# Kernel tuning notes

Hardware: AMD Instinct MI355X
Metric: run time of the kernel (lower is better)

The kernel has to match this reference:

```python
import jax, jax.numpy as jnp
import numpy as np

D_MODEL = 128
EXPAND = 8
D_INNER = EXPAND * D_MODEL            # 1024
HEADDIM = D_MODEL                     # headdim = int(in_channels*8/8)
NHEADS = D_INNER // HEADDIM           # 8
D_STATE = 128
D_CONV = 4
CONV_DIM = D_INNER + 2 * D_STATE      # 1280
D_IN_PROJ = 2 * D_INNER + 2 * D_STATE + NHEADS  # 2312
EPS = 1e-5
B_SZ, SEQ = 2, 2048


def setup_inputs() -> dict:
    key = jax.random.key(0)
    ks = jax.random.split(key, 16)
    n = jax.random.normal
    dt_init = jax.random.uniform(ks[4], (NHEADS,), minval=0.001, maxval=0.1)
    return dict(
        hidden_states=n(ks[0], (B_SZ, SEQ, D_MODEL), jnp.float32),
        w_in=n(ks[1], (D_IN_PROJ, D_MODEL), jnp.float32) / np.float32(np.sqrt(D_MODEL)),
        conv_w=n(ks[2], (CONV_DIM, D_CONV), jnp.float32) / np.float32(np.sqrt(D_CONV)),
        conv_b=n(ks[3], (CONV_DIM,), jnp.float32) * 0.01,
        dt_bias=jnp.log(jnp.expm1(dt_init)),  # inverse-softplus init (official)
        A_log=jnp.log(jax.random.uniform(ks[5], (NHEADS,), minval=1.0, maxval=16.0)),
        D_skip=jnp.ones((NHEADS,), jnp.float32),
        gnorm_w=jnp.ones((D_INNER,), jnp.float32),
        w_out=n(ks[6], (D_MODEL, D_INNER), jnp.float32) / np.float32(np.sqrt(D_INNER)),
        ln1_w=jnp.ones((D_MODEL,), jnp.float32),
        ln1_b=jnp.zeros((D_MODEL,), jnp.float32),
        ln2_w=jnp.ones((D_MODEL,), jnp.float32),
        ln2_b=jnp.zeros((D_MODEL,), jnp.float32),
        mlp_w=n(ks[7], (D_MODEL, D_MODEL), jnp.float32) / np.float32(np.sqrt(D_MODEL)),
        mlp_b=jnp.zeros((D_MODEL,), jnp.float32),
    )


def _layer_norm(x, w, b):
    m = x.mean(-1, keepdims=True)
    xc = x - m
    v = (xc * xc).mean(-1, keepdims=True)
    return xc * jax.lax.rsqrt(v + EPS) * w + b


def _mixer(u, w_in, conv_w, conv_b, dt_bias, A_log, D_skip, gnorm_w, w_out):
    b, l, _ = u.shape
    zxbcdt = u @ w_in.T                                    # (b,l,2312)
    z = zxbcdt[..., :D_INNER]                              # gate
    xBC = zxbcdt[..., D_INNER:D_INNER + CONV_DIM]
    dt = jax.nn.softplus(zxbcdt[..., -NHEADS:] + dt_bias)  # (b,l,h)
    # depthwise causal conv1d + SiLU
    xc = jnp.pad(xBC.swapaxes(1, 2), ((0, 0), (0, 0), (D_CONV - 1, 0)))
    xc = jax.lax.conv_general_dilated(xc, conv_w[:, None, :], (1,), 'VALID',
                                      feature_group_count=CONV_DIM)
    xBC = jax.nn.silu((xc + conv_b[None, :, None]).swapaxes(1, 2))
    x = xBC[..., :D_INNER].reshape(b, l, NHEADS, HEADDIM)  # (b,l,h,p)
    Bm = xBC[..., D_INNER:D_INNER + D_STATE]               # (b,l,n), ngroups=1
    Cm = xBC[..., D_INNER + D_STATE:]                      # (b,l,n)
    A = -jnp.exp(A_log)                                    # (h,)
    dA = jnp.exp(dt * A)                                   # (b,l,h)

    def step(S, inp):
        dA_t, dt_t, B_t, C_t, x_t = inp
        S = S * dA_t[:, :, None, None] + jnp.einsum('bh,bhp,bn->bhpn', dt_t, x_t, B_t)
        return S, jnp.einsum('bhpn,bn->bhp', S, C_t)

    S0 = jnp.zeros((b, NHEADS, HEADDIM, D_STATE), u.dtype)
    _, ys = jax.lax.scan(step, S0, (dA.swapaxes(0, 1), dt.swapaxes(0, 1),
                                    Bm.swapaxes(0, 1), Cm.swapaxes(0, 1),
                                    x.swapaxes(0, 1)))
    y = ys.swapaxes(0, 1) + D_skip[None, None, :, None] * x  # skip connection
    y = y.reshape(b, l, D_INNER) * jax.nn.silu(z)            # gated RMSNorm
    y = y * jax.lax.rsqrt((y * y).mean(-1, keepdims=True) + EPS) * gnorm_w
    return y @ w_out.T


def reference(hidden_states, w_in, conv_w, conv_b, dt_bias, A_log, D_skip,
              gnorm_w, w_out, ln1_w, ln1_b, ln2_w, ln2_b, mlp_w, mlp_b):
    residual = hidden_states
    h = _layer_norm(residual, ln1_w, ln1_b)
    h = _mixer(h, w_in, conv_w, conv_b, dt_bias, A_log, D_skip, gnorm_w, w_out)
    residual = h + residual
    h = _layer_norm(residual, ln2_w, ln2_b)
    return h @ mlp_w.T + mlp_b
```

## Files before the change

### kernel.cpp

```cpp
#include <hip/hip_runtime.h>
#include <hip/hip_bf16.h>

#define B_SZ 2
#define SEQ 2048
#define DMODEL 128
#define DINNER 1024
#define NHEADS 8
#define HEADDIM 128
#define DSTATE 128
#define CONVDIM 1280
#define NPROJ 2304
#define NTOK (B_SZ*SEQ)
#define CHUNK 64
#define NCHUNK (SEQ/CHUNK)
#define LDT 72

using bf16_t = __hip_bfloat16;
using short8 = __attribute__((ext_vector_type(8))) short;
using short4v= __attribute__((ext_vector_type(4))) short;
using f32x4  = __attribute__((ext_vector_type(4))) float;

__device__ __forceinline__ float silu_f(float x) { return x / (1.f + expf(-x)); }
__device__ __forceinline__ float bf2f(short s) {
    unsigned u = ((unsigned)(unsigned short)s) << 16;
    return __uint_as_float(u);
}
__device__ __forceinline__ short f2bf_s(float f) {
    bf16_t h = __float2bfloat16(f);
    return *(short*)&h;
}

__global__ __launch_bounds__(128) void head_fused(
        const float* __restrict__ hidden,
        const float* __restrict__ ln1_w, const float* __restrict__ ln1_b,
        const float* __restrict__ w_in,
        const float* __restrict__ dt_bias, const float* __restrict__ A_log,
        bf16_t* __restrict__ h_bf, float* __restrict__ dtb, float* __restrict__ ldAb,
        const float* __restrict__ wa, int na, const float* __restrict__ wb, int nb,
        const float* __restrict__ wc, int nc,
        bf16_t* __restrict__ oa, bf16_t* __restrict__ ob, bf16_t* __restrict__ oc) {
    int blk = blockIdx.x;
    if (blk >= NTOK) {
        int i = (blk - NTOK) * 128 + threadIdx.x;
        if (i < na) oa[i] = __float2bfloat16(wa[i]);
        else if (i < na + nb) ob[i - na] = __float2bfloat16(wb[i - na]);
        else if (i < na + nb + nc) oc[i - na - nb] = __float2bfloat16(wc[i - na - nb]);
        return;
    }
    int m = blk, t = threadIdx.x;
    __shared__ float red[128];
    __shared__ float sred[2][8];
    float v = hidden[(size_t)m*DMODEL + t];
    red[t] = v; __syncthreads();
    for (int s = 64; s > 0; s >>= 1) { if (t < s) red[t] += red[t+s]; __syncthreads(); }
    float mean = red[0] * (1.f/128.f);
    __syncthreads();
    float xc = v - mean;
    red[t] = xc * xc; __syncthreads();
    for (int s = 64; s > 0; s >>= 1) { if (t < s) red[t] += red[t+s]; __syncthreads(); }
    float var = red[0] * (1.f/128.f);
    float o = xc * rsqrtf(var + 1e-5f) * ln1_w[t] + ln1_b[t];
    h_bf[(size_t)m*DMODEL + t] = __float2bfloat16(o);
    int wave = t >> 6, lane = t & 63;
#pragma unroll
    for (int hd = 0; hd < NHEADS; hd++) {
        float p = o * w_in[(size_t)(NPROJ + hd)*DMODEL + t];
#pragma unroll
        for (int d = 1; d < 64; d <<= 1) p += __shfl_xor(p, d, 64);
        if (lane == 0) sred[wave][hd] = p;
    }
    __syncthreads();
    if (t < NHEADS) {
        float s = sred[0][t] + sred[1][t] + dt_bias[t];
        float dtv = (s > 20.f) ? s : log1pf(expf(s));
        float Av = -expf(A_log[t]);
        dtb[m*NHEADS + t] = dtv;
        ldAb[m*NHEADS + t] = dtv * Av;
    }
}

__global__ __launch_bounds__(256) void gemm_bf(const bf16_t* __restrict__ A,
                                               const bf16_t* __restrict__ W,
                                               bf16_t* __restrict__ C,
                                               int M, int N, int K) {
    int tid = threadIdx.x;
    int wave = tid >> 6, lane = tid & 63;
    int m0 = blockIdx.x * 64 + wave * 16;
    int n0 = blockIdx.y * 64;
    int lr = lane & 15, quad = lane >> 4;
    f32x4 acc[4];
#pragma unroll
    for (int j = 0; j < 4; j++) acc[j] = (f32x4){0.f, 0.f, 0.f, 0.f};
    for (int k0 = 0; k0 < K; k0 += 32) {
        short8 a = *(const short8*)(A + (size_t)(m0 + lr)*K + k0 + quad*8);
#pragma unroll
        for (int j = 0; j < 4; j++) {
            short8 b = *(const short8*)(W + (size_t)(n0 + j*16 + lr)*K + k0 + quad*8);
            acc[j] = __builtin_amdgcn_mfma_f32_16x16x32_bf16(a, b, acc[j], 0, 0, 0);
        }
    }
#pragma unroll
    for (int j = 0; j < 4; j++)
#pragma unroll
        for (int r = 0; r < 4; r++) {
            int row = m0 + quad*4 + r;
            int col = n0 + j*16 + lr;
            C[(size_t)row*N + col] = __float2bfloat16(acc[j][r]);
        }
}

__global__ __launch_bounds__(256) void conv_silu(const bf16_t* __restrict__ zxb,
                                                 const float* __restrict__ conv_w,
                                                 const float* __restrict__ conv_b,
                                                 bf16_t* __restrict__ xBCb) {
    int idx = blockIdx.x * 256 + threadIdx.x;
    if (idx >= NTOK * CONVDIM / 4) return;
    int c4 = (idx % (CONVDIM/4)) * 4;
    int m  = idx / (CONVDIM/4);
    int b = m >> 11, l = m & (SEQ - 1);
    float acc[4];
    f32x4 wv[4];
#pragma unroll
    for (int j = 0; j < 4; j++) {
        acc[j] = conv_b[c4 + j];
        wv[j] = *(const f32x4*)(conv_w + (c4 + j)*4);
    }
#pragma unroll
    for (int k = 0; k < 4; k++) {
        int ll = l - 3 + k;
        if (ll >= 0) {
            short4v v = *(const short4v*)(zxb + (size_t)(b*SEQ + ll)*NPROJ + DINNER + c4);
#pragma unroll
            for (int j = 0; j < 4; j++) acc[j] += bf2f(v[j]) * wv[j][k];
        }
    }
    short4v res;
#pragma unroll
    for (int j = 0; j < 4; j++) res[j] = f2bf_s(silu_f(acc[j]));
    *(short4v*)(xBCb + (size_t)m*CONVDIM + c4) = res;
}

__global__ __launch_bounds__(256) void scanA_mfma(const bf16_t* __restrict__ xBCb,
                                                  const float* __restrict__ dt,
                                                  const float* __restrict__ ldA,
                                                  bf16_t* __restrict__ Sloc,
                                                  float* __restrict__ Pbuf) {
    int bid = blockIdx.x;
    int c = bid & 31, hd = (bid >> 5) & 7, b = bid >> 8;
    int t = threadIdx.x, wave = t >> 6, lane = t & 63;
    int lr = lane & 15, quad = lane >> 4;
    __shared__ bf16_t XT[128*LDT];
    __shared__ bf16_t BT[128*LDT];
    __shared__ float ws[CHUNK];
    int m0tok = b*SEQ + c*CHUNK;
    if (t < 64) {
        float L = ldA[(m0tok + t)*NHEADS + hd];
#pragma unroll
        for (int d = 1; d < 64; d <<= 1) {
            float u = __shfl_up(L, d, 64);
            if (lane >= d) L += u;
        }
        float Ltot = __shfl(L, 63, 64);
        ws[t] = expf(Ltot - L) * dt[(m0tok + t)*NHEADS + hd];
        if (t == 63) Pbuf[bid] = expf(Ltot);
    }
    __syncthreads();
#pragma unroll 4
    for (int i = 0; i < 32; i++) {
        int idx = i*256 + t;
        int tt = idx >> 7, p = idx & 127;
        const bf16_t* row = xBCb + (size_t)(m0tok + tt)*CONVDIM;
        float xv = bf2f(*(const short*)&row[hd*HEADDIM + p]);
        XT[p*LDT + tt] = __float2bfloat16(xv * ws[tt]);
        BT[p*LDT + tt] = row[DINNER + p];
    }
    __syncthreads();
    int m0w = wave * 32;
    f32x4 acc[2][8];
#pragma unroll
    for (int mi = 0; mi < 2; mi++)
#pragma unroll
        for (int ni = 0; ni < 8; ni++) acc[mi][ni] = (f32x4){0.f,0.f,0.f,0.f};
#pragma unroll
    for (int k0 = 0; k0 < 64; k0 += 32) {
        short8 a[2];
#pragma unroll
        for (int mi = 0; mi < 2; mi++)
            a[mi] = *(const short8*)&XT[(m0w + mi*16 + lr)*LDT + k0 + quad*8];
#pragma unroll
        for (int ni = 0; ni < 8; ni++) {
            short8 bb = *(const short8*)&BT[(ni*16 + lr)*LDT + k0 + quad*8];
#pragma unroll
            for (int mi = 0; mi < 2; mi++)
                acc[mi][ni] = __builtin_amdgcn_mfma_f32_16x16x32_bf16(a[mi], bb, acc[mi][ni], 0, 0, 0);
        }
    }
    bf16_t* outp = Sloc + (size_t)bid * 16384;
#pragma unroll
    for (int mi = 0; mi < 2; mi++)
#pragma unroll
        for (int ni = 0; ni < 8; ni++)
#pragma unroll
            for (int r = 0; r < 4; r++) {
                int p = m0w + mi*16 + quad*4 + r;
                int n = ni*16 + lr;
                outp[p*128 + n] = __float2bfloat16(acc[mi][ni][r]);
            }
}

__global__ __launch_bounds__(256) void scanB(const bf16_t* __restrict__ Sloc,
                                             bf16_t* __restrict__ Sini,
                                             const float* __restrict__ Pbuf) {
    int bid = blockIdx.x;
    int bh = bid >> 5, slice = bid & 31;
    int t = threadIdx.x;
    int off = slice*512 + t*2;
    size_t base = (size_t)bh * NCHUNK * 16384;
    float run0 = 0.f, run1 = 0.f;
    for (int cc = 0; cc < NCHUNK; cc++) {
        unsigned raw = *(const unsigned*)(Sloc + base + (size_t)cc*16384 + off);
        float P = Pbuf[bh*NCHUNK + cc];
        unsigned o0 = (unsigned)(unsigned short)f2bf_s(run0);
        unsigned o1 = (unsigned)(unsigned short)f2bf_s(run1);
        *(unsigned*)(Sini + base + (size_t)cc*16384 + off) = o0 | (o1 << 16);
        run0 = run0*P + bf2f((short)(raw & 0xffff));
        run1 = run1*P + bf2f((short)(raw >> 16));
    }
}

__global__ __launch_bounds__(256) void scanC_mfma(const bf16_t* __restrict__ xBCb,
                                                  const float* __restrict__ dt,
                                                  const float* __restrict__ ldA,
                                                  const bf16_t* __restrict__ Sini,
                                                  const float* __restrict__ Dskip,
                                                  float* __restrict__ ybuf) {
    int bid = blockIdx.x;
    int c = bid & 31, hd = (bid >> 5) & 7, b = bid >> 8;
    int t = threadIdx.x, wave = t >> 6, lane = t & 63;
    int lr = lane & 15, quad = lane >> 4;
    __shared__ bf16_t XT[128*LDT];
    __shared__ bf16_t Mlds[64*LDT];
    __shared__ float Ls[CHUNK], dts[CHUNK];
    int m0tok = b*SEQ + c*CHUNK;
    if (t < 64) {
        float L = ldA[(m0tok + t)*NHEADS + hd];
#pragma unroll
        for (int d = 1; d < 64; d <<= 1) {
            float u = __shfl_up(L, d, 64);
            if (lane >= d) L += u;
        }
        Ls[t] = L;
        dts[t] = dt[(m0tok + t)*NHEADS + hd];
    }
#pragma unroll 4
    for (int i = 0; i < 32; i++) {
        int idx = i*256 + t;
        int tt = idx >> 7, p = idx & 127;
        XT[p*LDT + tt] = xBCb[(size_t)(m0tok + tt)*CONVDIM + hd*HEADDIM + p];
    }
    __syncthreads();
    const bf16_t* Crow = xBCb + (size_t)m0tok*CONVDIM + DINNER + DSTATE;
    const bf16_t* Brow = xBCb + (size_t)m0tok*CONVDIM + DINNER;
    f32x4 g[4];
#pragma unroll
    for (int si = 0; si < 4; si++) g[si] = (f32x4){0.f,0.f,0.f,0.f};
#pragma unroll
    for (int k0 = 0; k0 < 128; k0 += 32) {
        short8 a = *(const short8*)(Crow + (size_t)(wave*16 + lr)*CONVDIM + k0 + quad*8);
#pragma unroll
        for (int si = 0; si < 4; si++) {
            short8 bb = *(const short8*)(Brow + (size_t)(si*16 + lr)*CONVDIM + k0 + quad*8);
            g[si] = __builtin_amdgcn_mfma_f32_16x16x32_bf16(a, bb, g[si], 0, 0, 0);
        }
    }
#pragma unroll
    for (int si = 0; si < 4; si++)
#pragma unroll
        for (int r = 0; r < 4; r++) {
            int tt = wave*16 + quad*4 + r;
            int ss = si*16 + lr;
            float v = (ss <= tt) ? g[si][r] * expf(Ls[tt] - Ls[ss]) * dts[ss] : 0.f;
            Mlds[tt*LDT + ss] = __float2bfloat16(v);
        }
    __syncthreads();
    int p0 = wave * 32;
    f32x4 acc[4][2];
#pragma unroll
    for (int mi = 0; mi < 4; mi++)
#pragma unroll
        for (int ni = 0; ni < 2; ni++) acc[mi][ni] = (f32x4){0.f,0.f,0.f,0.f};
    const bf16_t* Sb = Sini + (size_t)bid * 16384;
#pragma unroll
    for (int k0 = 0; k0 < 128; k0 += 32) {
        short8 aC[4];
#pragma unroll
        for (int mi = 0; mi < 4; mi++)
            aC[mi] = *(const short8*)(Crow + (size_t)(mi*16 + lr)*CONVDIM + k0 + quad*8);
#pragma unroll
        for (int ni = 0; ni < 2; ni++) {
            short8 bb = *(const short8*)(Sb + (size_t)(p0 + ni*16 + lr)*128 + k0 + quad*8);
#pragma unroll
            for (int mi = 0; mi < 4; mi++)
                acc[mi][ni] = __builtin_amdgcn_mfma_f32_16x16x32_bf16(aC[mi], bb, acc[mi][ni], 0, 0, 0);
        }
    }
#pragma unroll
    for (int mi = 0; mi < 4; mi++) {
        float el[4];
#pragma unroll
        for (int r = 0; r < 4; r++) el[r] = expf(Ls[mi*16 + quad*4 + r]);
#pragma unroll
        for (int ni = 0; ni < 2; ni++)
#pragma unroll
            for (int r = 0; r < 4; r++) acc[mi][ni][r] *= el[r];
    }
#pragma unroll
    for (int k0 = 0; k0 < 64; k0 += 32) {
        short8 aM[4];
#pragma unroll
        for (int mi = 0; mi < 4; mi++)
            aM[mi] = *(const short8*)&Mlds[(mi*16 + lr)*LDT + k0 + quad*8];
#pragma unroll
        for (int ni = 0; ni < 2; ni++) {
            short8 bb = *(const short8*)&XT[(p0 + ni*16 + lr)*LDT + k0 + quad*8];
#pragma unroll
            for (int mi = 0; mi < 4; mi++)
                acc[mi][ni] = __builtin_amdgcn_mfma_f32_16x16x32_bf16(aM[mi], bb, acc[mi][ni], 0, 0, 0);
        }
    }
    float dsk = Dskip[hd];
#pragma unroll
    for (int mi = 0; mi < 4; mi++)
#pragma unroll
        for (int ni = 0; ni < 2; ni++)
#pragma unroll
            for (int r = 0; r < 4; r++) {
                int tt = mi*16 + quad*4 + r;
                int pp = p0 + ni*16 + lr;
                float xv = bf2f(*(const short*)&XT[pp*LDT + tt]);
                int m = m0tok + tt;
                ybuf[(size_t)m*DINNER + hd*HEADDIM + pp] = acc[mi][ni][r] + dsk*xv;
            }
}

__global__ __launch_bounds__(256) void gate_out(const float* __restrict__ ybuf,
                                                const bf16_t* __restrict__ zxb,
                                                const float* __restrict__ gw,
                                                const bf16_t* __restrict__ Wb,
                                                float* __restrict__ mix) {
    int blk = blockIdx.x, t = threadIdx.x;
    int tok0 = blk * 16;
    int tt = t >> 4, cg = t & 15;
    int ch0 = cg * 64;
    __shared__ bf16_t A[16*1032];
    float vals[64];
    const float*  yr = ybuf + (size_t)(tok0 + tt)*DINNER + ch0;
    const bf16_t* zr = zxb  + (size_t)(tok0 + tt)*NPROJ  + ch0;
    float ss = 0.f;
#pragma unroll
    for (int i = 0; i < 64; i += 4) {
        f32x4 y = *(const f32x4*)(yr + i);
        short4v z = *(const short4v*)(zr + i);
#pragma unroll
        for (int r = 0; r < 4; r++) {
            float v = y[r] * silu_f(bf2f(z[r]));
            vals[i + r] = v; ss += v*v;
        }
    }
#pragma unroll
    for (int d = 1; d < 16; d <<= 1) ss += __shfl_xor(ss, d, 64);
    float rstd = rsqrtf(ss*(1.f/1024.f) + 1e-5f);
#pragma unroll
    for (int i = 0; i < 64; i += 4) {
        short4v pk;
#pragma unroll
        for (int r = 0; r < 4; r++) pk[r] = f2bf_s(vals[i+r]*rstd*gw[ch0+i+r]);
        *(short4v*)&A[tt*1032 + ch0 + i] = pk;
    }
    __syncthreads();
    int wave = t >> 6, lane = t & 63, lr = lane & 15, quad = lane >> 4;
    f32x4 acc[2];
    acc[0] = (f32x4){0.f,0.f,0.f,0.f}; acc[1] = (f32x4){0.f,0.f,0.f,0.f};
    for (int k0 = 0; k0 < 1024; k0 += 32) {
        short8 a = *(const short8*)&A[lr*1032 + k0 + quad*8];
#pragma unroll
        for (int j = 0; j < 2; j++) {
            int col = wave*32 + j*16 + lr;
            short8 bb = *(const short8*)(Wb + (size_t)col*DINNER + k0 + quad*8);
            acc[j] = __builtin_amdgcn_mfma_f32_16x16x32_bf16(a, bb, acc[j], 0, 0, 0);
        }
    }
#pragma unroll
    for (int j = 0; j < 2; j++)
#pragma unroll
        for (int r = 0; r < 4; r++) {
            int row = tok0 + quad*4 + r;
            int col = wave*32 + j*16 + lr;
            mix[(size_t)row*DMODEL + col] = acc[j][r];
        }
}

__global__ __launch_bounds__(256) void ln_mlp(const float* __restrict__ mix,
                                              const float* __restrict__ resid,
                                              const float* __restrict__ w,
                                              const float* __restrict__ b,
                                              const bf16_t* __restrict__ Wm,
                                              const float* __restrict__ mb,
                                              float* __restrict__ out) {
    int blk = blockIdx.x, t = threadIdx.x;
    int tok0 = blk * 16;
    int tt = t >> 4, cg = t & 15;
    int ch0 = cg * 8;
    __shared__ bf16_t A[16*136];
    const float* xr = mix   + (size_t)(tok0 + tt)*DMODEL + ch0;
    const float* rr = resid + (size_t)(tok0 + tt)*DMODEL + ch0;
    float v[8];
    {
        f32x4 x0 = *(const f32x4*)xr, x1 = *(const f32x4*)(xr + 4);
        f32x4 r0 = *(const f32x4*)rr, r1 = *(const f32x4*)(rr + 4);
#pragma unroll
        for (int r = 0; r < 4; r++) { v[r] = x0[r] + r0[r]; v[4+r] = x1[r] + r1[r]; }
    }
    float s = 0.f, sq = 0.f;
#pragma unroll
    for (int i = 0; i < 8; i++) { s += v[i]; sq += v[i]*v[i]; }
#pragma unroll
    for (int d = 1; d < 16; d <<= 1) { s += __shfl_xor(s, d, 64); sq += __shfl_xor(sq, d, 64); }
    float mean = s * (1.f/128.f);
    float var  = sq * (1.f/128.f) - mean*mean;
    float rstd = rsqrtf(var + 1e-5f);
    {
        short4v p0, p1;
#pragma unroll
        for (int r = 0; r < 4; r++) {
            p0[r] = f2bf_s((v[r]   - mean)*rstd*w[ch0+r]   + b[ch0+r]);
            p1[r] = f2bf_s((v[4+r] - mean)*rstd*w[ch0+4+r] + b[ch0+4+r]);
        }
        *(short4v*)&A[tt*136 + ch0]     = p0;
        *(short4v*)&A[tt*136 + ch0 + 4] = p1;
    }
    __syncthreads();
    int wave = t >> 6, lane = t & 63, lr = lane & 15, quad = lane >> 4;
    f32x4 acc[2];
    acc[0] = (f32x4){0.f,0.f,0.f,0.f}; acc[1] = (f32x4){0.f,0.f,0.f,0.f};
#pragma unroll
    for (int k0 = 0; k0 < 128; k0 += 32) {
        short8 a = *(const short8*)&A[lr*136 + k0 + quad*8];
#pragma unroll
        for (int j = 0; j < 2; j++) {
            int col = wave*32 + j*16 + lr;
            short8 bb = *(const short8*)(Wm + (size_t)col*DMODEL + k0 + quad*8);
            acc[j] = __builtin_amdgcn_mfma_f32_16x16x32_bf16(a, bb, acc[j], 0, 0, 0);
        }
    }
#pragma unroll
    for (int j = 0; j < 2; j++)
#pragma unroll
        for (int r = 0; r < 4; r++) {
            int row = tok0 + quad*4 + r;
            int col = wave*32 + j*16 + lr;
            out[(size_t)row*DMODEL + col] = acc[j][r] + mb[col];
        }
}

extern "C" void kernel_launch(void* const* d_in, const int* in_sizes, int n_in,
                              void* d_out, int out_size, void* d_ws, size_t ws_size,
                              hipStream_t stream) {
    const float* hidden  = (const float*)d_in[0];
    const float* w_in    = (const float*)d_in[1];
    const float* conv_w  = (const float*)d_in[2];
    const float* conv_b  = (const float*)d_in[3];
    const float* dt_bias = (const float*)d_in[4];
    const float* A_log   = (const float*)d_in[5];
    const float* D_skip  = (const float*)d_in[6];
    const float* gnorm_w = (const float*)d_in[7];
    const float* w_out   = (const float*)d_in[8];
    const float* ln1_w   = (const float*)d_in[9];
    const float* ln1_b   = (const float*)d_in[10];
    const float* ln2_w   = (const float*)d_in[11];
    const float* ln2_b   = (const float*)d_in[12];
    const float* mlp_w   = (const float*)d_in[13];
    const float* mlp_b   = (const float*)d_in[14];
    float* out = (float*)d_out;

    char* ws = (char*)d_ws;
    size_t off = 0;
    auto alloc = [&](size_t bytes) -> void* {
        void* p = ws + off;
        off = (off + bytes + 255) & ~(size_t)255;
        return p;
    };
    bf16_t* h_bf   = (bf16_t*)alloc((size_t)NTOK*DMODEL*2);
    bf16_t* w_in_bf= (bf16_t*)alloc((size_t)NPROJ*DMODEL*2);
    bf16_t* w_out_bf=(bf16_t*)alloc((size_t)DMODEL*DINNER*2);
    bf16_t* mlp_bf = (bf16_t*)alloc((size_t)DMODEL*DMODEL*2);
    bf16_t* zx_bf  = (bf16_t*)alloc((size_t)NTOK*NPROJ*2);
    bf16_t* xBCb   = (bf16_t*)alloc((size_t)NTOK*CONVDIM*2);
    float*  dtb    = (float*) alloc((size_t)NTOK*NHEADS*4);
    float*  ldAb   = (float*) alloc((size_t)NTOK*NHEADS*4);
    bf16_t* Sloc   = (bf16_t*)alloc((size_t)B_SZ*NHEADS*NCHUNK*16384*2);
    bf16_t* Sini   = (bf16_t*)alloc((size_t)B_SZ*NHEADS*NCHUNK*16384*2);
    float*  Pbuf   = (float*) alloc((size_t)B_SZ*NHEADS*NCHUNK*4);
    float*  ybuf   = (float*) alloc((size_t)NTOK*DINNER*4);
    float*  mix    = (float*) alloc((size_t)NTOK*DMODEL*4);
    (void)ws_size; (void)in_sizes; (void)n_in; (void)out_size;

    {
        int na = NPROJ*DMODEL, nb = DMODEL*DINNER, nc = DMODEL*DMODEL;
        int castBlocks = (na + nb + nc + 127) / 128;
        head_fused<<<NTOK + castBlocks, 128, 0, stream>>>(
            hidden, ln1_w, ln1_b, w_in, dt_bias, A_log, h_bf, dtb, ldAb,
            w_in, na, w_out, nb, mlp_w, nc, w_in_bf, w_out_bf, mlp_bf);
    }
    gemm_bf<<<dim3(NTOK/64, NPROJ/64), 256, 0, stream>>>(h_bf, w_in_bf, zx_bf,
                                                         NTOK, NPROJ, DMODEL);
    conv_silu<<<((size_t)NTOK*CONVDIM/4 + 255)/256, 256, 0, stream>>>(zx_bf, conv_w, conv_b, xBCb);
    scanA_mfma<<<B_SZ*NHEADS*NCHUNK, 256, 0, stream>>>(xBCb, dtb, ldAb, Sloc, Pbuf);
    scanB<<<B_SZ*NHEADS*NCHUNK, 256, 0, stream>>>(Sloc, Sini, Pbuf);
    scanC_mfma<<<B_SZ*NHEADS*NCHUNK, 256, 0, stream>>>(xBCb, dtb, ldAb, Sini, D_skip, ybuf);
    gate_out<<<NTOK/16, 256, 0, stream>>>(ybuf, zx_bf, gnorm_w, w_out_bf, mix);
    ln_mlp<<<NTOK/16, 256, 0, stream>>>(mix, hidden, ln2_w, ln2_b, mlp_bf, mlp_b, out);
}
```

Measured before the change: 184.2 us.

## Fuse gate_out with LN2+MLP, vectorize scan staging loads, shuffle-based LN1 reductions

Merges the gated-RMSNorm/out-projection kernel with the second LayerNorm and MLP kernel, keeping the mixer output in shared memory instead of writing and re-reading a global buffer, which saves one launch. The transposed staging of x and B in scanA/scanC now uses 16-byte vector loads per token row instead of scalar bf16 loads. The LN1 reductions in head_fused use wave shuffles instead of a shared-memory tree with many barriers. The fused kernel uses more shared memory per block.

```diff
diff --git a/kernel.cpp b/kernel.cpp
--- a/kernel.cpp
+++ b/kernel.cpp
@@ -48,20 +48,25 @@
         return;
     }
     int m = blk, t = threadIdx.x;
-    __shared__ float red[128];
+    int wave = t >> 6, lane = t & 63;
+    __shared__ float sA[2], sB[2];
     __shared__ float sred[2][8];
     float v = hidden[(size_t)m*DMODEL + t];
-    red[t] = v; __syncthreads();
-    for (int s = 64; s > 0; s >>= 1) { if (t < s) red[t] += red[t+s]; __syncthreads(); }
-    float mean = red[0] * (1.f/128.f);
-    __syncthreads();
+    float s = v;
+#pragma unroll
+    for (int d = 1; d < 64; d <<= 1) s += __shfl_xor(s, d, 64);
+    if (lane == 0) sA[wave] = s;
+    __syncthreads();
+    float mean = (sA[0] + sA[1]) * (1.f/128.f);
     float xc = v - mean;
-    red[t] = xc * xc; __syncthreads();
-    for (int s = 64; s > 0; s >>= 1) { if (t < s) red[t] += red[t+s]; __syncthreads(); }
-    float var = red[0] * (1.f/128.f);
+    float q = xc * xc;
+#pragma unroll
+    for (int d = 1; d < 64; d <<= 1) q += __shfl_xor(q, d, 64);
+    if (lane == 0) sB[wave] = q;
+    __syncthreads();
+    float var = (sB[0] + sB[1]) * (1.f/128.f);
     float o = xc * rsqrtf(var + 1e-5f) * ln1_w[t] + ln1_b[t];
     h_bf[(size_t)m*DMODEL + t] = __float2bfloat16(o);
-    int wave = t >> 6, lane = t & 63;
 #pragma unroll
     for (int hd = 0; hd < NHEADS; hd++) {
         float p = o * w_in[(size_t)(NPROJ + hd)*DMODEL + t];
@@ -71,8 +76,8 @@
     }
     __syncthreads();
     if (t < NHEADS) {
-        float s = sred[0][t] + sred[1][t] + dt_bias[t];
-        float dtv = (s > 20.f) ? s : log1pf(expf(s));
+        float ssum = sred[0][t] + sred[1][t] + dt_bias[t];
+        float dtv = (ssum > 20.f) ? ssum : log1pf(expf(ssum));
         float Av = -expf(A_log[t]);
         dtb[m*NHEADS + t] = dtv;
         ldAb[m*NHEADS + t] = dtv * Av;
@@ -165,14 +170,20 @@
         if (t == 63) Pbuf[bid] = expf(Ltot);
     }
     __syncthreads();
-#pragma unroll 4
-    for (int i = 0; i < 32; i++) {
-        int idx = i*256 + t;
-        int tt = idx >> 7, p = idx & 127;
+#pragma unroll
+    for (int i = 0; i < 4; i++) {
+        int tt = t & 63;
+        int pg = i*4 + (t >> 6);
         const bf16_t* row = xBCb + (size_t)(m0tok + tt)*CONVDIM;
-        float xv = bf2f(*(const short*)&row[hd*HEADDIM + p]);
-        XT[p*LDT + tt] = __float2bfloat16(xv * ws[tt]);
-        BT[p*LDT + tt] = row[DINNER + p];
+        short8 xv = *(const short8*)(row + hd*HEADDIM + pg*8);
+        short8 bv = *(const short8*)(row + DINNER + pg*8);
+        float w = ws[tt];
+#pragma unroll
+        for (int j = 0; j < 8; j++) {
+            XT[(pg*8 + j)*LDT + tt] = __float2bfloat16(bf2f(xv[j]) * w);
+            short sv = bv[j];
+            BT[(pg*8 + j)*LDT + tt] = *(bf16_t*)&sv;
+        }
     }
     __syncthreads();
     int m0w = wave * 32;
@@ -252,11 +263,16 @@
         Ls[t] = L;
         dts[t] = dt[(m0tok + t)*NHEADS + hd];
     }
-#pragma unroll 4
-    for (int i = 0; i < 32; i++) {
-        int idx = i*256 + t;
-        int tt = idx >> 7, p = idx & 127;
-        XT[p*LDT + tt] = xBCb[(size_t)(m0tok + tt)*CONVDIM + hd*HEADDIM + p];
+#pragma unroll
+    for (int i = 0; i < 4; i++) {
+        int tt = t & 63;
+        int pg = i*4 + (t >> 6);
+        short8 xv = *(const short8*)(xBCb + (size_t)(m0tok + tt)*CONVDIM + hd*HEADDIM + pg*8);
+#pragma unroll
+        for (int j = 0; j < 8; j++) {
+            short sv = xv[j];
+            XT[(pg*8 + j)*LDT + tt] = *(bf16_t*)&sv;
+        }
     }
     __syncthreads();
     const bf16_t* Crow = xBCb + (size_t)m0tok*CONVDIM + DINNER + DSTATE;
@@ -343,16 +359,22 @@
             }
 }
 
-__global__ __launch_bounds__(256) void gate_out(const float* __restrict__ ybuf,
-                                                const bf16_t* __restrict__ zxb,
-                                                const float* __restrict__ gw,
-                                                const bf16_t* __restrict__ Wb,
-                                                float* __restrict__ mix) {
+__global__ __launch_bounds__(256) void gate_out_mlp(const float* __restrict__ ybuf,
+                                                    const bf16_t* __restrict__ zxb,
+                                                    const float* __restrict__ gw,
+                                                    const bf16_t* __restrict__ Wb,
+                                                    const float* __restrict__ resid,
+                                                    const float* __restrict__ w2,
+                                                    const float* __restrict__ b2,
+                                                    const bf16_t* __restrict__ Wm,
+                                                    const float* __restrict__ mb,
+                                                    float* __restrict__ out) {
     int blk = blockIdx.x, t = threadIdx.x;
     int tok0 = blk * 16;
     int tt = t >> 4, cg = t & 15;
     int ch0 = cg * 64;
     __shared__ bf16_t A[16*1032];
+    __shared__ float mixs[16*132];
     float vals[64];
     const float*  yr = ybuf + (size_t)(tok0 + tt)*DINNER + ch0;
     const bf16_t* zr = zxb  + (size_t)(tok0 + tt)*NPROJ  + ch0;
@@ -393,73 +415,59 @@
 #pragma unroll
     for (int j = 0; j < 2; j++)
 #pragma unroll
+        for (int r = 0; r < 4; r++)
+            mixs[(quad*4 + r)*132 + wave*32 + j*16 + lr] = acc[j][r];
+    __syncthreads();
+    bf16_t* A2 = A;
+    int ch8 = cg * 8;
+    const float* rr = resid + (size_t)(tok0 + tt)*DMODEL + ch8;
+    float v2[8];
+    {
+        f32x4 r0 = *(const f32x4*)rr, r1 = *(const f32x4*)(rr + 4);
+#pragma unroll
+        for (int r = 0; r < 4; r++) {
+            v2[r]   = mixs[tt*132 + ch8 + r]     + r0[r];
+            v2[4+r] = mixs[tt*132 + ch8 + 4 + r] + r1[r];
+        }
+    }
+    float s2 = 0.f, sq = 0.f;
+#pragma unroll
+    for (int i = 0; i < 8; i++) { s2 += v2[i]; sq += v2[i]*v2[i]; }
+#pragma unroll
+    for (int d = 1; d < 16; d <<= 1) { s2 += __shfl_xor(s2, d, 64); sq += __shfl_xor(sq, d, 64); }
+    float mean = s2 * (1.f/128.f);
+    float var  = sq * (1.f/128.f) - mean*mean;
+    float rstd2 = rsqrtf(var + 1e-5f);
+    {
+        short4v p0, p1;
+#pragma unroll
+        for (int r = 0; r < 4; r++) {
+            p0[r] = f2bf_s((v2[r]   - mean)*rstd2*w2[ch8+r]   + b2[ch8+r]);
+            p1[r] = f2bf_s((v2[4+r] - mean)*rstd2*w2[ch8+4+r] + b2[ch8+4+r]);
+        }
+        *(short4v*)&A2[tt*136 + ch8]     = p0;
+        *(short4v*)&A2[tt*136 + ch8 + 4] = p1;
+    }
+    __syncthreads();
+    f32x4 acc2[2];
+    acc2[0] = (f32x4){0.f,0.f,0.f,0.f}; acc2[1] = (f32x4){0.f,0.f,0.f,0.f};
+#pragma unroll
+    for (int k0 = 0; k0 < 128; k0 += 32) {
+        short8 a = *(const short8*)&A2[lr*136 + k0 + quad*8];
+#pragma unroll
+        for (int j = 0; j < 2; j++) {
+            int col = wave*32 + j*16 + lr;
+            short8 bb = *(const short8*)(Wm + (size_t)col*DMODEL + k0 + quad*8);
+            acc2[j] = __builtin_amdgcn_mfma_f32_16x16x32_bf16(a, bb, acc2[j], 0, 0, 0);
+        }
+    }
+#pragma unroll
+    for (int j = 0; j < 2; j++)
+#pragma unroll
         for (int r = 0; r < 4; r++) {
             int row = tok0 + quad*4 + r;
             int col = wave*32 + j*16 + lr;
-            mix[(size_t)row*DMODEL + col] = acc[j][r];
-        }
-}
-
-__global__ __launch_bounds__(256) void ln_mlp(const float* __restrict__ mix,
-                                              const float* __restrict__ resid,
-                                              const float* __restrict__ w,
-                                              const float* __restrict__ b,
-                                              const bf16_t* __restrict__ Wm,
-                                              const float* __restrict__ mb,
-                                              float* __restrict__ out) {
-    int blk = blockIdx.x, t = threadIdx.x;
-    int tok0 = blk * 16;
-    int tt = t >> 4, cg = t & 15;
-    int ch0 = cg * 8;
-    __shared__ bf16_t A[16*136];
-    const float* xr = mix   + (size_t)(tok0 + tt)*DMODEL + ch0;
-    const float* rr = resid + (size_t)(tok0 + tt)*DMODEL + ch0;
-    float v[8];
-    {
-        f32x4 x0 = *(const f32x4*)xr, x1 = *(const f32x4*)(xr + 4);
-        f32x4 r0 = *(const f32x4*)rr, r1 = *(const f32x4*)(rr + 4);
-#pragma unroll
-        for (int r = 0; r < 4; r++) { v[r] = x0[r] + r0[r]; v[4+r] = x1[r] + r1[r]; }
-    }
-    float s = 0.f, sq = 0.f;
-#pragma unroll
-    for (int i = 0; i < 8; i++) { s += v[i]; sq += v[i]*v[i]; }
-#pragma unroll
-    for (int d = 1; d < 16; d <<= 1) { s += __shfl_xor(s, d, 64); sq += __shfl_xor(sq, d, 64); }
-    float mean = s * (1.f/128.f);
-    float var  = sq * (1.f/128.f) - mean*mean;
-    float rstd = rsqrtf(var + 1e-5f);
-    {
-        short4v p0, p1;
-#pragma unroll
-        for (int r = 0; r < 4; r++) {
-            p0[r] = f2bf_s((v[r]   - mean)*rstd*w[ch0+r]   + b[ch0+r]);
-            p1[r] = f2bf_s((v[4+r] - mean)*rstd*w[ch0+4+r] + b[ch0+4+r]);
-        }
-        *(short4v*)&A[tt*136 + ch0]     = p0;
-        *(short4v*)&A[tt*136 + ch0 + 4] = p1;
-    }
-    __syncthreads();
-    int wave = t >> 6, lane = t & 63, lr = lane & 15, quad = lane >> 4;
-    f32x4 acc[2];
-    acc[0] = (f32x4){0.f,0.f,0.f,0.f}; acc[1] = (f32x4){0.f,0.f,0.f,0.f};
-#pragma unroll
-    for (int k0 = 0; k0 < 128; k0 += 32) {
-        short8 a = *(const short8*)&A[lr*136 + k0 + quad*8];
-#pragma unroll
-        for (int j = 0; j < 2; j++) {
-            int col = wave*32 + j*16 + lr;
-            short8 bb = *(const short8*)(Wm + (size_t)col*DMODEL + k0 + quad*8);
-            acc[j] = __builtin_amdgcn_mfma_f32_16x16x32_bf16(a, bb, acc[j], 0, 0, 0);
-        }
-    }
-#pragma unroll
-    for (int j = 0; j < 2; j++)
-#pragma unroll
-        for (int r = 0; r < 4; r++) {
-            int row = tok0 + quad*4 + r;
-            int col = wave*32 + j*16 + lr;
-            out[(size_t)row*DMODEL + col] = acc[j][r] + mb[col];
+            out[(size_t)row*DMODEL + col] = acc2[j][r] + mb[col];
         }
 }
 
@@ -502,7 +510,6 @@
     bf16_t* Sini   = (bf16_t*)alloc((size_t)B_SZ*NHEADS*NCHUNK*16384*2);
     float*  Pbuf   = (float*) alloc((size_t)B_SZ*NHEADS*NCHUNK*4);
     float*  ybuf   = (float*) alloc((size_t)NTOK*DINNER*4);
-    float*  mix    = (float*) alloc((size_t)NTOK*DMODEL*4);
     (void)ws_size; (void)in_sizes; (void)n_in; (void)out_size;
 
     {
@@ -518,6 +525,6 @@
     scanA_mfma<<<B_SZ*NHEADS*NCHUNK, 256, 0, stream>>>(xBCb, dtb, ldAb, Sloc, Pbuf);
     scanB<<<B_SZ*NHEADS*NCHUNK, 256, 0, stream>>>(Sloc, Sini, Pbuf);
     scanC_mfma<<<B_SZ*NHEADS*NCHUNK, 256, 0, stream>>>(xBCb, dtb, ldAb, Sini, D_skip, ybuf);
-    gate_out<<<NTOK/16, 256, 0, stream>>>(ybuf, zx_bf, gnorm_w, w_out_bf, mix);
-    ln_mlp<<<NTOK/16, 256, 0, stream>>>(mix, hidden, ln2_w, ln2_b, mlp_bf, mlp_b, out);
-}
+    gate_out_mlp<<<NTOK/16, 256, 0, stream>>>(ybuf, zx_bf, gnorm_w, w_out_bf,
+                                              hidden, ln2_w, ln2_b, mlp_bf, mlp_b, out);
+}
```

After: 181.4 us. Within noise of the previous version (-1.6%).
